# Kernel tuning notes

Measured on AMD Instinct MI355X. Metric: run time of the kernel, lower is better.

## Reference

```python
import jax, jax.numpy as jnp
import numpy as np

B, M, H = 8, 2048, 1024


def setup_inputs() -> dict:
    key = jax.random.key(0)
    k0, k1, k2, k3, k4 = jax.random.split(key, 5)
    return {
        "query": jax.random.normal(k0, (B, M, H), dtype=jnp.float32),
        "key": jax.random.normal(k1, (B, M, H), dtype=jnp.float32),
        "span": jax.random.uniform(k2, (B, M, 2), dtype=jnp.float32),
        "value": jax.random.normal(k3, (B, M, H), dtype=jnp.float32),
        "key_pe": jax.random.normal(k4, (1, H, M), dtype=jnp.float32),
    }


def reference(query, key, span, value, key_pe):
    # Faithful to the source's returned value:
    #   attn_cont (span-gathered version) is overwritten by the dense q @ k^T,
    #   and the scaled/softmaxed `attn` (content + positional) is computed but
    #   NEVER used for the output. The module returns attn_cont @ value with
    #   no scaling and no softmax. span / key_pe do not affect the output.
    attn_cont = jnp.einsum('bmh,bnh->bmn', query, key)  # [B, M, M]
    out = jnp.matmul(attn_cont, value)                   # [B, M, H]
    return out
```

## Files before the change

### kernel.cpp

```cpp
#include <hip/hip_runtime.h>
#include <hip/hip_bf16.h>

typedef __attribute__((ext_vector_type(4))) float f32x4;
typedef __attribute__((ext_vector_type(8))) short bf16x8;
typedef __attribute__((ext_vector_type(2))) unsigned int u32x2;
typedef unsigned short u16;
typedef unsigned int u32;


__device__ __forceinline__ u16 f2bf(float f) {
  union { float f; unsigned int u; } v;
  v.f = f;
  unsigned int r = (v.u + 0x7fffu + ((v.u >> 16) & 1u)) >> 16;
  return (u16)r;
}

__device__ __forceinline__ u32 pk2(float a, float b) {
  u32 r;
  asm("v_cvt_pk_bf16_f32 %0, %1, %2" : "=v"(r) : "v"(a), "v"(b));
  return r;
}

__device__ __forceinline__ void async16(const void* g, const void* l) {
  __builtin_amdgcn_global_load_lds(
      (const __attribute__((address_space(1))) unsigned int*)(unsigned long)g,
      (__attribute__((address_space(3))) unsigned int*)(unsigned int)(unsigned long)l,
      16, 0, 0);
}

__device__ __forceinline__ void bar() {
  asm volatile("" ::: "memory");
  __builtin_amdgcn_s_barrier();
  asm volatile("" ::: "memory");
}

#define WAIT_LGKM0() asm volatile("s_waitcnt lgkmcnt(0)" ::: "memory")
#define WAIT_VM0()   asm volatile("s_waitcnt vmcnt(0)" ::: "memory")
#define G8(r) ((((r) >> 3) ^ (r)) & 7)


__global__ __launch_bounds__(256) void cvt_kv(const float* __restrict__ Kin,
                                              const float* __restrict__ Vin,
                                              u16* __restrict__ Kt,
                                              u16* __restrict__ Vt) {
  __shared__ u16 tile[64][68];
  const int z = blockIdx.z;
  const int bsel = z >> 1;
  const float* in = (z & 1) ? Kin : Vin;
  u16* out = (z & 1) ? Kt : Vt;
  const long bo = (long)bsel * 2048 * 1024;
  const int r0 = blockIdx.y * 64;
  const int c0 = blockIdx.x * 64;
  const int t = threadIdx.x;
  const int tr = t >> 4;
  const int tc4 = (t & 15) * 4;

#pragma unroll
  for (int i = 0; i < 4; ++i) {
    int r = i * 16 + tr;
    f32x4 v = *(const f32x4*)(in + bo + (long)(r0 + r) * 1024 + c0 + tc4);
    tile[tc4 + 0][r] = f2bf(v.x);
    tile[tc4 + 1][r] = f2bf(v.y);
    tile[tc4 + 2][r] = f2bf(v.z);
    tile[tc4 + 3][r] = f2bf(v.w);
  }
  __syncthreads();
#pragma unroll
  for (int i = 0; i < 4; ++i) {
    int c = i * 16 + tr;
    ushort4 u = *(const ushort4*)(&tile[c][tc4]);
    *(ushort4*)(out + bo + (long)(c0 + c) * 2048 + r0 + tc4) = u;
  }
}

__global__ __launch_bounds__(512, 2) void gemmA(const u16* __restrict__ Vt,
                                                const u16* __restrict__ Kt,
                                                u16* __restrict__ Pt) {
  __shared__ u16 As[2][256][64];
  __shared__ u16 Bs[2][128][64];

  const int bid = blockIdx.x;
  const int b = bid & 7;
  const int tile = bid >> 3;
  const int bn0 = (tile & 7) * 128;
  const int bm0 = (tile >> 3) * 256;

  const int tid = threadIdx.x;
  const int lane = tid & 63;
  const int wave = tid >> 6;
  const int wr = wave >> 2;
  const int wc = wave & 3;
  const int l16 = lane & 15;
  const int kh = lane >> 4;

  const char* Ab = (const char*)(Vt + (long)b * 1024 * 2048);
  const char* Bb = (const char*)(Kt + (long)b * 1024 * 2048);

  int aoff[4], boff[2];
#pragma unroll
  for (int i = 0; i < 4; ++i) {
    int u = tid + i * 512;
    int row = u >> 3, sl = (u & 7) ^ (row & 7);
    aoff[i] = (bm0 + row) * 4096 + sl * 16;
  }
#pragma unroll
  for (int i = 0; i < 2; ++i) {
    int u = tid + i * 512;
    int row = u >> 3, sl = (u & 7) ^ (row & 7);
    boff[i] = (bn0 + row) * 4096 + sl * 16;
  }

#define STG_A(buf)                                                          \
  {                                                                         \
    _Pragma("unroll") for (int i_ = 0; i_ < 4; ++i_) {                      \
      async16(Ab + aoff[i_], (char*)&As[buf][0][0] + (tid + i_ * 512) * 16);\
      aoff[i_] += 128;                                                      \
    }                                                                       \
  }
#define STG_B(buf)                                                          \
  {                                                                         \
    _Pragma("unroll") for (int i_ = 0; i_ < 2; ++i_) {                      \
      async16(Bb + boff[i_], (char*)&Bs[buf][0][0] + (tid + i_ * 512) * 16);\
      boff[i_] += 128;                                                      \
    }                                                                       \
  }

  int offA[2][4][2];
#pragma unroll
  for (int q = 0; q < 2; ++q)
#pragma unroll
    for (int f = 0; f < 4; ++f) {
      int r = q * 128 + wr * 64 + f * 16 + l16;
#pragma unroll
      for (int ks = 0; ks < 2; ++ks)
        offA[q][f][ks] = r * 64 + (((ks * 4 + kh) ^ (l16 & 7)) * 8);
    }
  int offB[2][2];
#pragma unroll
  for (int fn = 0; fn < 2; ++fn) {
    int r = fn * 64 + wc * 16 + l16;
#pragma unroll
    for (int ks = 0; ks < 2; ++ks)
      offB[fn][ks] = r * 64 + (((ks * 4 + kh) ^ (l16 & 7)) * 8);
  }

  f32x4 acc[8][2] = {};
  bf16x8 ar[4][2], br[2][2];

  STG_A(0); STG_B(0);
  WAIT_VM0();
  bar();

  const int NT = 32;
  for (int t = 0; t < NT; ++t) {
    const int cur = t & 1, nxt = cur ^ 1;
    const bool g = (t + 1 < NT);
    const u16* Abuf = &As[cur][0][0];
    const u16* Bbuf = &Bs[cur][0][0];

#pragma unroll
    for (int f = 0; f < 4; ++f)
#pragma unroll
      for (int ks = 0; ks < 2; ++ks)
        ar[f][ks] = *(const bf16x8*)(Abuf + offA[0][f][ks]);
#pragma unroll
    for (int fn = 0; fn < 2; ++fn)
#pragma unroll
      for (int ks = 0; ks < 2; ++ks)
        br[fn][ks] = *(const bf16x8*)(Bbuf + offB[fn][ks]);

    if (g) { STG_A(nxt); STG_B(nxt); }

    __builtin_amdgcn_s_setprio(1);
#pragma unroll
    for (int f = 0; f < 4; ++f)
#pragma unroll
      for (int n = 0; n < 2; ++n)
#pragma unroll
        for (int ks = 0; ks < 2; ++ks)
          acc[f][n] = __builtin_amdgcn_mfma_f32_16x16x32_bf16(
              ar[f][ks], br[n][ks], acc[f][n], 0, 0, 0);
    __builtin_amdgcn_s_setprio(0);

#pragma unroll
    for (int f = 0; f < 4; ++f)
#pragma unroll
      for (int ks = 0; ks < 2; ++ks)
        ar[f][ks] = *(const bf16x8*)(Abuf + offA[1][f][ks]);

    __builtin_amdgcn_s_setprio(1);
#pragma unroll
    for (int f = 0; f < 4; ++f)
#pragma unroll
      for (int n = 0; n < 2; ++n)
#pragma unroll
        for (int ks = 0; ks < 2; ++ks)
          acc[4 + f][n] = __builtin_amdgcn_mfma_f32_16x16x32_bf16(
              ar[f][ks], br[n][ks], acc[4 + f][n], 0, 0, 0);
    __builtin_amdgcn_s_setprio(0);

    if (g) WAIT_VM0();
    bar();
  }
#undef STG_A
#undef STG_B

  u16* Cb = Pt + (long)b * 1024 * 1024;
#pragma unroll
  for (int fm = 0; fm < 8; ++fm) {
    const int gm = bm0 + (fm >> 2) * 128 + wr * 64 + (fm & 3) * 16 + kh * 4;
#pragma unroll
    for (int fn = 0; fn < 2; ++fn) {
      const int gn = bn0 + fn * 64 + wc * 16 + l16;
#pragma unroll
      for (int r = 0; r < 4; ++r)
        Cb[(long)(gm + r) * 1024 + gn] = f2bf(acc[fm][fn][r]);
    }
  }
}

__global__ __launch_bounds__(512, 2) void gemmB(const float* __restrict__ Q,
                                                const u16* __restrict__ Pt,
                                                float* __restrict__ out) {
  __shared__ u16 As[2][256][64];
  __shared__ u16 Bs[2][2][128][64];

  const int bid = blockIdx.x;
  const int b = bid & 7;
  const int tile = bid >> 3;
  const int bn0 = (tile & 3) * 256;
  const int bm0 = (tile >> 2) * 256;

  const int tid = threadIdx.x;
  const int lane = tid & 63;
  const int wave = tid >> 6;
  const int wr = wave >> 2;
  const int wc = wave & 3;
  const int l16 = lane & 15;
  const int kh = lane >> 4;

  const int mrow = tid >> 4;
  const char* pQ = (const char*)(Q + (long)b * 2048 * 1024 +
                                 (long)(bm0 + mrow) * 1024 + (tid & 15) * 4);

  int qwo[8];
#pragma unroll
  for (int p = 0; p < 8; ++p) {
    int r = p * 32 + mrow;
    qwo[p] = r * 128 + ((((tid & 15) >> 1) ^ G8(r)) * 16) + (tid & 1) * 8;
  }

  int boff[2][2];
#pragma unroll
  for (int h = 0; h < 2; ++h)
#pragma unroll
    for (int i = 0; i < 2; ++i) {
      int u = tid + i * 512;
      int row = u >> 3, sl = (u & 7) ^ (row & 7);
      boff[h][i] = (bn0 + h * 128 + row) * 2048 + sl * 16;
    }
  const char* PtB = (const char*)(Pt + (long)b * 1024 * 1024);

  int offA[2][4][2];
#pragma unroll
  for (int q = 0; q < 2; ++q)
#pragma unroll
    for (int f = 0; f < 4; ++f) {
      int r = q * 128 + wr * 64 + f * 16 + l16;
#pragma unroll
      for (int ks = 0; ks < 2; ++ks)
        offA[q][f][ks] = r * 64 + (((ks * 4 + kh) ^ G8(r)) * 8);
    }
  int offBf[2][2];
#pragma unroll
  for (int g_ = 0; g_ < 2; ++g_) {
    int r = wc * 32 + g_ * 16 + l16;
#pragma unroll
    for (int ks = 0; ks < 2; ++ks)
      offBf[g_][ks] = r * 64 + (((ks * 4 + kh) ^ (l16 & 7)) * 8);
  }

#define STG_PT(h, buf)                                                      \
  {                                                                         \
    _Pragma("unroll") for (int i_ = 0; i_ < 2; ++i_) {                      \
      async16(PtB + boff[h][i_],                                            \
              (char*)&Bs[buf][h][0][0] + (tid + i_ * 512) * 16);            \
      boff[h][i_] += 128;                                                   \
    }                                                                       \
  }

  f32x4 acc[8][4] = {};
  f32x4 qv[8];
  bf16x8 ar[4][2], br[4][2];

#pragma unroll
  for (int p = 0; p < 8; ++p) qv[p] = *(const f32x4*)(pQ + p * 131072);
  STG_PT(0, 0);
  STG_PT(1, 0);
  {
    char* dA = (char*)&As[0][0][0];
#pragma unroll
    for (int p = 0; p < 8; ++p) {
      u32x2 v; v.x = pk2(qv[p].x, qv[p].y); v.y = pk2(qv[p].z, qv[p].w);
      *(u32x2*)(dA + qwo[p]) = v;
    }
  }
  pQ += 256;
  WAIT_VM0();
  WAIT_LGKM0();
  bar();

  const int NT = 16;
  for (int t = 0; t < NT; ++t) {
    const int cur = t & 1, nxt = cur ^ 1;
    const bool g = (t + 1 < NT);
    const u16* Ab = &As[cur][0][0];

#pragma unroll
    for (int f = 0; f < 4; ++f)
#pragma unroll
      for (int ks = 0; ks < 2; ++ks)
        ar[f][ks] = *(const bf16x8*)(Ab + offA[0][f][ks]);
#pragma unroll
    for (int qn = 0; qn < 2; ++qn)
#pragma unroll
      for (int g_ = 0; g_ < 2; ++g_)
#pragma unroll
        for (int ks = 0; ks < 2; ++ks)
          br[qn * 2 + g_][ks] =
              *(const bf16x8*)(&Bs[cur][qn][0][0] + offBf[g_][ks]);

    if (g) {
#pragma unroll
      for (int p = 0; p < 8; ++p) qv[p] = *(const f32x4*)(pQ + p * 131072);
      STG_PT(0, nxt);
      STG_PT(1, nxt);
    }

    __builtin_amdgcn_s_setprio(1);
#pragma unroll
    for (int f = 0; f < 4; ++f)
#pragma unroll
      for (int n = 0; n < 4; ++n)
#pragma unroll
        for (int ks = 0; ks < 2; ++ks)
          acc[f][n] = __builtin_amdgcn_mfma_f32_16x16x32_bf16(
              ar[f][ks], br[n][ks], acc[f][n], 0, 0, 0);
    __builtin_amdgcn_s_setprio(0);

#pragma unroll
    for (int f = 0; f < 4; ++f)
#pragma unroll
      for (int ks = 0; ks < 2; ++ks)
        ar[f][ks] = *(const bf16x8*)(Ab + offA[1][f][ks]);

    if (g) {
      char* dA = (char*)&As[nxt][0][0];
#pragma unroll
      for (int p = 0; p < 8; ++p) {
        u32x2 v; v.x = pk2(qv[p].x, qv[p].y); v.y = pk2(qv[p].z, qv[p].w);
        *(u32x2*)(dA + qwo[p]) = v;
      }
      pQ += 256;
    }

    __builtin_amdgcn_s_setprio(1);
#pragma unroll
    for (int f = 0; f < 4; ++f)
#pragma unroll
      for (int n = 0; n < 4; ++n)
#pragma unroll
        for (int ks = 0; ks < 2; ++ks)
          acc[4 + f][n] = __builtin_amdgcn_mfma_f32_16x16x32_bf16(
              ar[f][ks], br[n][ks], acc[4 + f][n], 0, 0, 0);
    __builtin_amdgcn_s_setprio(0);

    if (g) WAIT_VM0();
    WAIT_LGKM0();
    bar();
  }

  float* Cf = out + (long)b * 2048 * 1024;
#pragma unroll
  for (int fm = 0; fm < 8; ++fm) {
    const int gm = bm0 + (fm >> 2) * 128 + wr * 64 + (fm & 3) * 16 + kh * 4;
#pragma unroll
    for (int fn = 0; fn < 4; ++fn) {
      const int gn = bn0 + (fn >> 1) * 128 + wc * 32 + (fn & 1) * 16 + l16;
#pragma unroll
      for (int r = 0; r < 4; ++r)
        Cf[(long)(gm + r) * 1024 + gn] = acc[fm][fn][r];
    }
  }
#undef STG_PT
}


extern "C" void kernel_launch(void* const* d_in, const int* in_sizes, int n_in,
                              void* d_out, int out_size, void* d_ws, size_t ws_size,
                              hipStream_t stream) {
  const float* Q  = (const float*)d_in[0];
  const float* Kf = (const float*)d_in[1];
  const float* V  = (const float*)d_in[3];
  float* out = (float*)d_out;

  char* ws = (char*)d_ws;
  u16* Vt = (u16*)(ws);
  u16* Kt = (u16*)(ws + (size_t)32 * 1024 * 1024);
  u16* Pt = (u16*)(ws + (size_t)64 * 1024 * 1024);

  cvt_kv<<<dim3(16, 32, 16), 256, 0, stream>>>(Kf, V, Kt, Vt);

  gemmA<<<256, 512, 0, stream>>>(Vt, Kt, Pt);

  gemmB<<<256, 512, 0, stream>>>(Q, Pt, out);
}
```

Measured before the change: 134.9 us.

## Pre-convert Q to bf16 and use k-chunked layouts for K/V and P

The conversion kernel now also turns Q into bf16 in a workspace buffer. K and V are written in a k-chunk-major layout of 8-element slabs instead of a padded 64x64 transpose, and gemmA's LDS tiles and intermediate P output follow that chunked layout. gemmB now reads bf16 Q through async global-to-LDS loads rather than loading fp32 and converting in registers, and uses smaller 256x128 tiles with twice as many blocks. This removes in-loop conversion and register pressure in gemmB, at the cost of an extra pass writing and re-reading Q through memory.

```diff
diff --git a/kernel.cpp b/kernel.cpp
--- a/kernel.cpp
+++ b/kernel.cpp
@@ -34,50 +34,70 @@
   asm volatile("" ::: "memory");
 }
 
-#define WAIT_LGKM0() asm volatile("s_waitcnt lgkmcnt(0)" ::: "memory")
-#define WAIT_VM0()   asm volatile("s_waitcnt vmcnt(0)" ::: "memory")
-#define G8(r) ((((r) >> 3) ^ (r)) & 7)
-
-
-__global__ __launch_bounds__(256) void cvt_kv(const float* __restrict__ Kin,
-                                              const float* __restrict__ Vin,
-                                              u16* __restrict__ Kt,
-                                              u16* __restrict__ Vt) {
-  __shared__ u16 tile[64][68];
-  const int z = blockIdx.z;
-  const int bsel = z >> 1;
-  const float* in = (z & 1) ? Kin : Vin;
-  u16* out = (z & 1) ? Kt : Vt;
-  const long bo = (long)bsel * 2048 * 1024;
-  const int r0 = blockIdx.y * 64;
-  const int c0 = blockIdx.x * 64;
+#define WAIT_VM0() asm volatile("s_waitcnt vmcnt(0)" ::: "memory")
+
+__global__ __launch_bounds__(256) void cvt_all(const float* __restrict__ Kin,
+                                               const float* __restrict__ Vin,
+                                               const float* __restrict__ Q,
+                                               u16* __restrict__ Kt,
+                                               u16* __restrict__ Vt,
+                                               u16* __restrict__ Qb) {
+  __shared__ char tile[16384];
+  const int z = blockIdx.y;
   const int t = threadIdx.x;
-  const int tr = t >> 4;
-  const int tc4 = (t & 15) * 4;
-
-#pragma unroll
-  for (int i = 0; i < 4; ++i) {
-    int r = i * 16 + tr;
-    f32x4 v = *(const f32x4*)(in + bo + (long)(r0 + r) * 1024 + c0 + tc4);
-    tile[tc4 + 0][r] = f2bf(v.x);
-    tile[tc4 + 1][r] = f2bf(v.y);
-    tile[tc4 + 2][r] = f2bf(v.z);
-    tile[tc4 + 3][r] = f2bf(v.w);
-  }
-  __syncthreads();
-#pragma unroll
-  for (int i = 0; i < 4; ++i) {
-    int c = i * 16 + tr;
-    ushort4 u = *(const ushort4*)(&tile[c][tc4]);
-    *(ushort4*)(out + bo + (long)(c0 + c) * 2048 + r0 + tc4) = u;
+
+  if (z < 16) {
+    const int bsel = z >> 1;
+    const float* in = (z & 1) ? Kin : Vin;
+    u16* out = (z & 1) ? Kt : Vt;
+    const long bo = (long)bsel * 2048 * 1024;
+    const int s = blockIdx.x;
+    const float* src = in + bo + (long)s * 8 * 1024;
+
+    f32x4 v[8];
+#pragma unroll
+    for (int i = 0; i < 8; ++i)
+      v[i] = *(const f32x4*)(src + i * 1024 + t * 4);
+
+#pragma unroll
+    for (int q = 0; q < 4; ++q) {
+      const int c = t * 4 + q;
+      const int val = c ^ ((c >> 3) & 7);
+      union { u32 w[4]; uint4 u4; } U;
+      U.w[0] = pk2(v[0][q], v[1][q]);
+      U.w[1] = pk2(v[2][q], v[3][q]);
+      U.w[2] = pk2(v[4][q], v[5][q]);
+      U.w[3] = pk2(v[6][q], v[7][q]);
+      *(uint4*)(tile + ((long)val << 4)) = U.u4;
+    }
+    __syncthreads();
+
+    u16* dst = out + bo + (long)s * 8192;
+#pragma unroll
+    for (int p = 0; p < 4; ++p) {
+      const int u = t + p * 256;
+      const int val = u ^ ((u >> 3) & 7);
+      uint4 r = *(const uint4*)(tile + ((long)val << 4));
+      *(uint4*)(dst + (long)u * 8) = r;
+    }
+  } else {
+    const int qb = z - 16;
+    const float* src = Q + (long)qb * 2048 * 1024 + (long)blockIdx.x * 8192;
+    u16* dst = Qb + (long)qb * 2048 * 1024 + (long)blockIdx.x * 8192;
+#pragma unroll
+    for (int i = 0; i < 8; ++i) {
+      f32x4 v = *(const f32x4*)(src + (t + i * 256) * 4);
+      u32x2 w; w.x = pk2(v.x, v.y); w.y = pk2(v.z, v.w);
+      *(u32x2*)(dst + (long)(t + i * 256) * 4) = w;
+    }
   }
 }
 
 __global__ __launch_bounds__(512, 2) void gemmA(const u16* __restrict__ Vt,
                                                 const u16* __restrict__ Kt,
                                                 u16* __restrict__ Pt) {
-  __shared__ u16 As[2][256][64];
-  __shared__ u16 Bs[2][128][64];
+  __shared__ u16 As[2][8][256][8];
+  __shared__ u16 Bs[2][8][128][8];
 
   const int bid = blockIdx.x;
   const int b = bid & 7;
@@ -100,49 +120,44 @@
 #pragma unroll
   for (int i = 0; i < 4; ++i) {
     int u = tid + i * 512;
-    int row = u >> 3, sl = (u & 7) ^ (row & 7);
-    aoff[i] = (bm0 + row) * 4096 + sl * 16;
+    aoff[i] = (u >> 8) * 16384 + (bm0 + (u & 255)) * 16;
   }
 #pragma unroll
   for (int i = 0; i < 2; ++i) {
     int u = tid + i * 512;
-    int row = u >> 3, sl = (u & 7) ^ (row & 7);
-    boff[i] = (bn0 + row) * 4096 + sl * 16;
-  }
-
-#define STG_A(buf)                                                          \
-  {                                                                         \
-    _Pragma("unroll") for (int i_ = 0; i_ < 4; ++i_) {                      \
-      async16(Ab + aoff[i_], (char*)&As[buf][0][0] + (tid + i_ * 512) * 16);\
-      aoff[i_] += 128;                                                      \
-    }                                                                       \
-  }
-#define STG_B(buf)                                                          \
-  {                                                                         \
-    _Pragma("unroll") for (int i_ = 0; i_ < 2; ++i_) {                      \
-      async16(Bb + boff[i_], (char*)&Bs[buf][0][0] + (tid + i_ * 512) * 16);\
-      boff[i_] += 128;                                                      \
-    }                                                                       \
+    boff[i] = (u >> 7) * 16384 + (bn0 + (u & 127)) * 16;
+  }
+
+#define STG_A(buf)                                                             \
+  {                                                                            \
+    _Pragma("unroll") for (int i_ = 0; i_ < 4; ++i_) {                         \
+      async16(Ab + aoff[i_], (char*)&As[buf][0][0][0] + (tid + i_ * 512) * 16);\
+      aoff[i_] += 131072;                                                      \
+    }                                                                          \
+  }
+#define STG_B(buf)                                                             \
+  {                                                                            \
+    _Pragma("unroll") for (int i_ = 0; i_ < 2; ++i_) {                         \
+      async16(Bb + boff[i_], (char*)&Bs[buf][0][0][0] + (tid + i_ * 512) * 16);\
+      boff[i_] += 131072;                                                      \
+    }                                                                          \
   }
 
   int offA[2][4][2];
 #pragma unroll
   for (int q = 0; q < 2; ++q)
 #pragma unroll
-    for (int f = 0; f < 4; ++f) {
-      int r = q * 128 + wr * 64 + f * 16 + l16;
-#pragma unroll
-      for (int ks = 0; ks < 2; ++ks)
-        offA[q][f][ks] = r * 64 + (((ks * 4 + kh) ^ (l16 & 7)) * 8);
-    }
+    for (int f = 0; f < 4; ++f)
+#pragma unroll
+      for (int ks = 0; ks < 2; ++ks)
+        offA[q][f][ks] =
+            (ks * 4 + kh) * 4096 + (q * 128 + wr * 64 + f * 16 + l16) * 16;
   int offB[2][2];
 #pragma unroll
-  for (int fn = 0; fn < 2; ++fn) {
-    int r = fn * 64 + wc * 16 + l16;
+  for (int fn = 0; fn < 2; ++fn)
 #pragma unroll
     for (int ks = 0; ks < 2; ++ks)
-      offB[fn][ks] = r * 64 + (((ks * 4 + kh) ^ (l16 & 7)) * 8);
-  }
+      offB[fn][ks] = (ks * 4 + kh) * 2048 + (fn * 64 + wc * 16 + l16) * 16;
 
   f32x4 acc[8][2] = {};
   bf16x8 ar[4][2], br[2][2];
@@ -155,8 +170,8 @@
   for (int t = 0; t < NT; ++t) {
     const int cur = t & 1, nxt = cur ^ 1;
     const bool g = (t + 1 < NT);
-    const u16* Abuf = &As[cur][0][0];
-    const u16* Bbuf = &Bs[cur][0][0];
+    const char* Abuf = (const char*)&As[cur][0][0][0];
+    const char* Bbuf = (const char*)&Bs[cur][0][0][0];
 
 #pragma unroll
     for (int f = 0; f < 4; ++f)
@@ -211,25 +226,25 @@
     const int gm = bm0 + (fm >> 2) * 128 + wr * 64 + (fm & 3) * 16 + kh * 4;
 #pragma unroll
     for (int fn = 0; fn < 2; ++fn) {
-      const int gn = bn0 + fn * 64 + wc * 16 + l16;
 #pragma unroll
       for (int r = 0; r < 4; ++r)
-        Cb[(long)(gm + r) * 1024 + gn] = f2bf(acc[fm][fn][r]);
-    }
-  }
-}
-
-__global__ __launch_bounds__(512, 2) void gemmB(const float* __restrict__ Q,
-                                                const u16* __restrict__ Pt,
+        Cb[(long)((bn0 >> 6) + fn) * 65536 + (long)(gm + r) * 64 +
+           wc * 16 + l16] = f2bf(acc[fm][fn][r]);
+    }
+  }
+}
+
+__global__ __launch_bounds__(512, 2) void gemmB(const u16* __restrict__ A,
+                                                const u16* __restrict__ Bt,
                                                 float* __restrict__ out) {
   __shared__ u16 As[2][256][64];
-  __shared__ u16 Bs[2][2][128][64];
+  __shared__ u16 Bs[2][128][64];
 
   const int bid = blockIdx.x;
   const int b = bid & 7;
   const int tile = bid >> 3;
-  const int bn0 = (tile & 3) * 256;
-  const int bm0 = (tile >> 2) * 256;
+  const int bn0 = (tile & 7) * 128;
+  const int bm0 = (tile >> 3) * 256;
 
   const int tid = threadIdx.x;
   const int lane = tid & 63;
@@ -239,27 +254,37 @@
   const int l16 = lane & 15;
   const int kh = lane >> 4;
 
-  const int mrow = tid >> 4;
-  const char* pQ = (const char*)(Q + (long)b * 2048 * 1024 +
-                                 (long)(bm0 + mrow) * 1024 + (tid & 15) * 4);
-
-  int qwo[8];
-#pragma unroll
-  for (int p = 0; p < 8; ++p) {
-    int r = p * 32 + mrow;
-    qwo[p] = r * 128 + ((((tid & 15) >> 1) ^ G8(r)) * 16) + (tid & 1) * 8;
-  }
-
-  int boff[2][2];
-#pragma unroll
-  for (int h = 0; h < 2; ++h)
-#pragma unroll
-    for (int i = 0; i < 2; ++i) {
-      int u = tid + i * 512;
-      int row = u >> 3, sl = (u & 7) ^ (row & 7);
-      boff[h][i] = (bn0 + h * 128 + row) * 2048 + sl * 16;
-    }
-  const char* PtB = (const char*)(Pt + (long)b * 1024 * 1024);
+  const char* Ab = (const char*)(A + (long)b * 2048 * 1024);
+  const char* Bb = (const char*)(Bt + (long)b * 1024 * 1024);
+
+  int aoff[4], boff[2];
+#pragma unroll
+  for (int i = 0; i < 4; ++i) {
+    int u = tid + i * 512;
+    int row = u >> 3, sl = (u & 7) ^ (row & 7);
+    aoff[i] = (bm0 + row) * 2048 + sl * 16;
+  }
+#pragma unroll
+  for (int i = 0; i < 2; ++i) {
+    int u = tid + i * 512;
+    int row = u >> 3, sl = (u & 7) ^ (row & 7);
+    boff[i] = (bn0 + row) * 128 + sl * 16;
+  }
+
+#define STG_A(buf)                                                          \
+  {                                                                         \
+    _Pragma("unroll") for (int i_ = 0; i_ < 4; ++i_) {                      \
+      async16(Ab + aoff[i_], (char*)&As[buf][0][0] + (tid + i_ * 512) * 16);\
+      aoff[i_] += 128;                                                      \
+    }                                                                       \
+  }
+#define STG_B(buf)                                                          \
+  {                                                                         \
+    _Pragma("unroll") for (int i_ = 0; i_ < 2; ++i_) {                      \
+      async16(Bb + boff[i_], (char*)&Bs[buf][0][0] + (tid + i_ * 512) * 16);\
+      boff[i_] += 131072;                                                   \
+    }                                                                       \
+  }
 
   int offA[2][4][2];
 #pragma unroll
@@ -269,79 +294,49 @@
       int r = q * 128 + wr * 64 + f * 16 + l16;
 #pragma unroll
       for (int ks = 0; ks < 2; ++ks)
-        offA[q][f][ks] = r * 64 + (((ks * 4 + kh) ^ G8(r)) * 8);
-    }
-  int offBf[2][2];
-#pragma unroll
-  for (int g_ = 0; g_ < 2; ++g_) {
-    int r = wc * 32 + g_ * 16 + l16;
+        offA[q][f][ks] = r * 64 + (((ks * 4 + kh) ^ (l16 & 7)) * 8);
+    }
+  int offB[2][2];
+#pragma unroll
+  for (int fn = 0; fn < 2; ++fn) {
+    int r = fn * 64 + wc * 16 + l16;
 #pragma unroll
     for (int ks = 0; ks < 2; ++ks)
-      offBf[g_][ks] = r * 64 + (((ks * 4 + kh) ^ (l16 & 7)) * 8);
-  }
-
-#define STG_PT(h, buf)                                                      \
-  {                                                                         \
-    _Pragma("unroll") for (int i_ = 0; i_ < 2; ++i_) {                      \
-      async16(PtB + boff[h][i_],                                            \
-              (char*)&Bs[buf][h][0][0] + (tid + i_ * 512) * 16);            \
-      boff[h][i_] += 128;                                                   \
-    }                                                                       \
-  }
-
-  f32x4 acc[8][4] = {};
-  f32x4 qv[8];
-  bf16x8 ar[4][2], br[4][2];
-
-#pragma unroll
-  for (int p = 0; p < 8; ++p) qv[p] = *(const f32x4*)(pQ + p * 131072);
-  STG_PT(0, 0);
-  STG_PT(1, 0);
-  {
-    char* dA = (char*)&As[0][0][0];
-#pragma unroll
-    for (int p = 0; p < 8; ++p) {
-      u32x2 v; v.x = pk2(qv[p].x, qv[p].y); v.y = pk2(qv[p].z, qv[p].w);
-      *(u32x2*)(dA + qwo[p]) = v;
-    }
-  }
-  pQ += 256;
+      offB[fn][ks] = r * 64 + (((ks * 4 + kh) ^ (l16 & 7)) * 8);
+  }
+
+  f32x4 acc[8][2] = {};
+  bf16x8 ar[4][2], br[2][2];
+
+  STG_A(0); STG_B(0);
   WAIT_VM0();
-  WAIT_LGKM0();
   bar();
 
   const int NT = 16;
   for (int t = 0; t < NT; ++t) {
     const int cur = t & 1, nxt = cur ^ 1;
     const bool g = (t + 1 < NT);
-    const u16* Ab = &As[cur][0][0];
-
-#pragma unroll
-    for (int f = 0; f < 4; ++f)
-#pragma unroll
-      for (int ks = 0; ks < 2; ++ks)
-        ar[f][ks] = *(const bf16x8*)(Ab + offA[0][f][ks]);
-#pragma unroll
-    for (int qn = 0; qn < 2; ++qn)
-#pragma unroll
-      for (int g_ = 0; g_ < 2; ++g_)
-#pragma unroll
-        for (int ks = 0; ks < 2; ++ks)
-          br[qn * 2 + g_][ks] =
-              *(const bf16x8*)(&Bs[cur][qn][0][0] + offBf[g_][ks]);
-
-    if (g) {
-#pragma unroll
-      for (int p = 0; p < 8; ++p) qv[p] = *(const f32x4*)(pQ + p * 131072);
-      STG_PT(0, nxt);
-      STG_PT(1, nxt);
-    }
+    const u16* Abuf = &As[cur][0][0];
+    const u16* Bbuf = &Bs[cur][0][0];
+
+#pragma unroll
+    for (int f = 0; f < 4; ++f)
+#pragma unroll
+      for (int ks = 0; ks < 2; ++ks)
+        ar[f][ks] = *(const bf16x8*)(Abuf + offA[0][f][ks]);
+#pragma unroll
+    for (int fn = 0; fn < 2; ++fn)
+#pragma unroll
+      for (int ks = 0; ks < 2; ++ks)
+        br[fn][ks] = *(const bf16x8*)(Bbuf + offB[fn][ks]);
+
+    if (g) { STG_A(nxt); STG_B(nxt); }
 
     __builtin_amdgcn_s_setprio(1);
 #pragma unroll
     for (int f = 0; f < 4; ++f)
 #pragma unroll
-      for (int n = 0; n < 4; ++n)
+      for (int n = 0; n < 2; ++n)
 #pragma unroll
         for (int ks = 0; ks < 2; ++ks)
           acc[f][n] = __builtin_amdgcn_mfma_f32_16x16x32_bf16(
@@ -352,23 +347,13 @@
     for (int f = 0; f < 4; ++f)
 #pragma unroll
       for (int ks = 0; ks < 2; ++ks)
-        ar[f][ks] = *(const bf16x8*)(Ab + offA[1][f][ks]);
-
-    if (g) {
-      char* dA = (char*)&As[nxt][0][0];
-#pragma unroll
-      for (int p = 0; p < 8; ++p) {
-        u32x2 v; v.x = pk2(qv[p].x, qv[p].y); v.y = pk2(qv[p].z, qv[p].w);
-        *(u32x2*)(dA + qwo[p]) = v;
-      }
-      pQ += 256;
-    }
+        ar[f][ks] = *(const bf16x8*)(Abuf + offA[1][f][ks]);
 
     __builtin_amdgcn_s_setprio(1);
 #pragma unroll
     for (int f = 0; f < 4; ++f)
 #pragma unroll
-      for (int n = 0; n < 4; ++n)
+      for (int n = 0; n < 2; ++n)
 #pragma unroll
         for (int ks = 0; ks < 2; ++ks)
           acc[4 + f][n] = __builtin_amdgcn_mfma_f32_16x16x32_bf16(
@@ -376,23 +361,23 @@
     __builtin_amdgcn_s_setprio(0);
 
     if (g) WAIT_VM0();
-    WAIT_LGKM0();
     bar();
   }
+#undef STG_A
+#undef STG_B
 
   float* Cf = out + (long)b * 2048 * 1024;
 #pragma unroll
   for (int fm = 0; fm < 8; ++fm) {
     const int gm = bm0 + (fm >> 2) * 128 + wr * 64 + (fm & 3) * 16 + kh * 4;
 #pragma unroll
-    for (int fn = 0; fn < 4; ++fn) {
-      const int gn = bn0 + (fn >> 1) * 128 + wc * 32 + (fn & 1) * 16 + l16;
+    for (int fn = 0; fn < 2; ++fn) {
+      const int gn = bn0 + fn * 64 + wc * 16 + l16;
 #pragma unroll
       for (int r = 0; r < 4; ++r)
         Cf[(long)(gm + r) * 1024 + gn] = acc[fm][fn][r];
     }
   }
-#undef STG_PT
 }
 
 
@@ -408,10 +393,11 @@
   u16* Vt = (u16*)(ws);
   u16* Kt = (u16*)(ws + (size_t)32 * 1024 * 1024);
   u16* Pt = (u16*)(ws + (size_t)64 * 1024 * 1024);
-
-  cvt_kv<<<dim3(16, 32, 16), 256, 0, stream>>>(Kf, V, Kt, Vt);
+  u16* Qb = (u16*)(ws + (size_t)80 * 1024 * 1024);
+
+  cvt_all<<<dim3(256, 24), 256, 0, stream>>>(Kf, V, Q, Kt, Vt, Qb);
 
   gemmA<<<256, 512, 0, stream>>>(Vt, Kt, Pt);
 
-  gemmB<<<256, 512, 0, stream>>>(Q, Pt, out);
-}
+  gemmB<<<512, 512, 0, stream>>>(Qb, Pt, out);
+}
```

After: 130.8 us (median of 2 runs). 1.03x faster.
